# Kernel optimization log

Hardware: AMD Instinct MI355X
Metric: run time of the kernel (lower is better)

The kernel has to match this reference:

```python
import jax, jax.numpy as jnp
import numpy as np

GL16 = [5, 3, 3, 3, 3, 3, 5, 5, 5, 11, 3, 3, 3, 3, 3, 12]  # sum 73
GL7 = [5, 9, 9, 25, 9, 9, 12]  # sum 78
BN_EPS = 1e-5
LRELU_SLOPE = 0.01


def setup_inputs() -> dict:
    key = jax.random.key(0)
    ks = jax.random.split(key, 32)
    B = 65536
    u = lambda k, shp, s: jax.random.uniform(k, shp, minval=-s, maxval=s)
    inp = {}
    inp['x'] = jax.random.normal(ks[0], (B, 310), dtype=jnp.float32)
    # learned adjacency (convert_dis_m(get_ini_dis_m(), 9) placeholder)
    inp['adj'] = jax.random.normal(ks[1], (62, 62), dtype=jnp.float32) * 0.1
    s5 = 1.0 / np.sqrt(5.0)
    inp['lgcn_w'] = u(ks[2], (5, 5), s5)
    inp['lgcn_b'] = u(ks[3], (5,), s5)
    # ChannelAttentionMPL (frequency, C=5) conv1d k=1 weights [out,in]
    inp['ca1_w1'] = jax.random.normal(ks[4], (32, 5)) * 0.3
    inp['ca1_w2'] = jax.random.normal(ks[5], (5, 32)) * 0.1
    # ChannelAttentionMPL (channel, C=62)
    inp['ca2_w1'] = jax.random.normal(ks[6], (32, 62)) * 0.1
    inp['ca2_w2'] = jax.random.normal(ks[7], (62, 32)) * 0.1
    # MesoLayer weights [5,10]
    inp['meso1_w'] = u(ks[8], (5, 10), 1.0 / np.sqrt(78.0))
    inp['meso2_w'] = u(ks[9], (5, 10), 1.0 / np.sqrt(78.0))
    # graphpool.feature_trans index maps (channel gathers into 62 channels)
    inp['idx16'] = jax.random.randint(ks[10], (73,), 0, 62, dtype=jnp.int32)
    inp['idx7'] = jax.random.randint(ks[11], (78,), 0, 62, dtype=jnp.int32)
    # MLP head 735->256->128->64 with eval-mode BatchNorm params
    def lin(ka, kb, fin, fout):
        s = 1.0 / np.sqrt(fin)
        return u(ka, (fin, fout), s), u(kb, (fout,), s)
    inp['w1'], inp['b1'] = lin(ks[12], ks[13], 735, 256)
    inp['w2'], inp['b2'] = lin(ks[14], ks[15], 256, 128)
    inp['w3'], inp['b3'] = lin(ks[16], ks[17], 128, 64)
    for i, (nm, d) in enumerate([('1', 256), ('2', 128), ('3', 64)]):
        inp['g' + nm] = 1.0 + 0.1 * jax.random.normal(ks[18 + 3 * i], (d,))
        inp['be' + nm] = 0.1 * jax.random.normal(ks[19 + 3 * i], (d,))
        inp['m' + nm] = 0.05 * jax.random.normal(ks[20 + 3 * i], (d,))
        inp['v' + nm] = jnp.ones((d,), dtype=jnp.float32)
    return inp


def channel_attention(x, w1, w2):
    # x: [B, C, L]; SE-style attention with avg+max pooling over L
    avg = jnp.mean(x, axis=2)            # [B, C]
    mx = jnp.max(x, axis=2)              # [B, C]
    def mlp(z):
        return jax.nn.relu(z @ w1.T) @ w2.T   # [B, C]
    att = jax.nn.sigmoid(mlp(avg) + mlp(mx))[:, :, None]  # [B, C, 1]
    return x + att * x, att


def meso(feat, idx, weight, graph_list):
    # feat: [B, 62, 5]; gather channels then per-subgraph attention pooling
    f = feat[:, idx]                     # [B, L, 5]
    outs = []
    h = 0
    for n in graph_list:                 # fixed small structural loop
        sub = jax.lax.dynamic_slice_in_dim(f, h, n, axis=1)  # [B, n, 5]
        fw = jnp.einsum('bjg,gh->bjh', sub, weight)          # [B, n, 10]
        # sum_i (fw @ fw^T)[b,j,i] == fw[b,j,:] . sum_i fw[b,i,:]
        scores = jnp.einsum('bjh,bh->bj', fw, jnp.sum(fw, axis=1))  # [B, n]
        att = jax.nn.softmax(scores, axis=1)
        outs.append(jnp.einsum('bj,bjg->bg', att, sub))      # [B, 5]
        h += n
    return jnp.stack(outs, axis=1)       # [B, S, 5]


def _forward(x, adj, lgcn_w, lgcn_b, ca1_w1, ca1_w2, ca2_w1, ca2_w2,
             meso1_w, meso2_w, idx16, idx7,
             w1, b1, g1, be1, m1, v1,
             w2, b2, g2, be2, m2, v2,
             w3, b3, g3, be3, m3, v3):
    B = x.shape[0]
    h = x.reshape(B, 5, 62).transpose(0, 2, 1)                   # [B, 62, 5]
    wf = jnp.einsum('bij,jd->bid', h, lgcn_w)
    h = jnp.einsum('ij,bjd->bid', adj, wf) + lgcn_b              # LocalLayer
    residual = h
    hx = h.transpose(0, 2, 1)                                    # [B, 5, 62]
    x_flat = hx.reshape(B, -1)                                   # [B, 310]
    out, att1 = channel_attention(hx, ca1_w1, ca1_w2)            # [B, 5, 62]
    out, att2 = channel_attention(out.transpose(0, 2, 1), ca2_w1, ca2_w2)  # [B,62,5]
    x1 = meso(residual, idx16, meso1_w, GL16).transpose(0, 2, 1).reshape(B, -1)  # [B, 80]
    x3 = meso(residual, idx7, meso2_w, GL7).transpose(0, 2, 1).reshape(B, -1)    # [B, 35]
    out_flat = out.transpose(0, 2, 1).reshape(B, -1)             # [B, 310]
    cat = jnp.concatenate([x_flat, out_flat, x1, x3], axis=1)    # [B, 735]

    def block(z, w, b, g, be, m, v):
        y = z @ w + b
        y = (y - m) / jnp.sqrt(v + BN_EPS) * g + be              # eval BN
        return jnp.where(y > 0, y, LRELU_SLOPE * y)              # LeakyReLU

    y = block(cat, w1, b1, g1, be1, m1, v1)
    y = block(y, w2, b2, g2, be2, m2, v2)
    y = block(y, w3, b3, g3, be3, m3, v3)
    return y, att1, att2


def reference(x, adj, lgcn_w, lgcn_b, ca1_w1, ca1_w2, ca2_w1, ca2_w2,
              meso1_w, meso2_w, idx16, idx7,
              w1, b1, w2, b2, w3, b3,
              g1, be1, m1, v1, g2, be2, m2, v2, g3, be3, m3, v3):
    return _forward(x, adj, lgcn_w, lgcn_b, ca1_w1, ca1_w2, ca2_w1, ca2_w2,
                    meso1_w, meso2_w, idx16, idx7,
                    w1, b1, g1, be1, m1, v1,
                    w2, b2, g2, be2, m2, v2,
                    w3, b3, g3, be3, m3, v3)
```

## Files before the change

### kernel.cpp

```cpp
#include <hip/hip_runtime.h>
#include <math.h>

#define BN_EPS 1e-5f
#define SLOPE 0.01f

typedef _Float16 f16;
typedef _Float16 f16x8 __attribute__((ext_vector_type(8)));
typedef float f32x4 __attribute__((ext_vector_type(4)));

__device__ __constant__ int c_g16_st[16] = {0,5,8,11,14,17,20,25,30,35,46,49,52,55,58,61};
__device__ __constant__ int c_g16_n[16]  = {5,3,3,3,3,3,5,5,5,11,3,3,3,3,3,12};
__device__ __constant__ int c_g7_st[7]   = {0,5,14,23,48,57,66};
__device__ __constant__ int c_g7_n[7]    = {5,9,9,25,9,9,12};

__device__ __forceinline__ float lrelu(float y) { return y > 0.f ? y : SLOPE * y; }

template<int T, int G, int BASE>
__device__ void meso_part(const int* __restrict__ st_arr, const int* __restrict__ n_arr,
                          int lane, long b, const float* h, const int* __restrict__ idxa,
                          const float* mw, float* fwbuf, float* scbuf,
                          f16* __restrict__ catb)
{
  const int team = lane / T, slot = lane - team * T;
  int st = 0, n = 0;
  if (team < G) { st = st_arr[team]; n = n_arr[team]; }
  float sp[10] = {0,0,0,0,0,0,0,0,0,0};
  if (team < G) {
    for (int j = slot; j < n; j += T) {
      int ri = idxa[st + j];
      float sv[5];
      #pragma unroll
      for (int g = 0; g < 5; ++g) sv[g] = h[ri*8 + g];
      #pragma unroll
      for (int t = 0; t < 10; ++t) {
        float f = sv[0]*mw[t] + sv[1]*mw[10+t] + sv[2]*mw[20+t] + sv[3]*mw[30+t] + sv[4]*mw[40+t];
        fwbuf[(st+j)*10 + t] = f;
        sp[t] += f;
      }
    }
  }
  #pragma unroll
  for (int off = 1; off < T; off <<= 1) {
    #pragma unroll
    for (int t = 0; t < 10; ++t) sp[t] += __shfl_xor(sp[t], off);
  }
  __syncthreads();
  if (team < G) {
    for (int j = slot; j < n; j += T) {
      float sc = 0.f;
      #pragma unroll
      for (int t = 0; t < 10; ++t) sc += fwbuf[(st+j)*10 + t] * sp[t];
      scbuf[st + j] = sc;
    }
  }
  __syncthreads();
  float po[5] = {0,0,0,0,0};
  if (team < G) {
    float mx = -1e30f;
    for (int jj = 0; jj < n; ++jj) mx = fmaxf(mx, scbuf[st + jj]);
    float sum = 0.f;
    for (int jj = 0; jj < n; ++jj) sum += expf(scbuf[st + jj] - mx);
    float inv = 1.f / sum;
    for (int j = slot; j < n; j += T) {
      float a = expf(scbuf[st + j] - mx) * inv;
      int ri = idxa[st + j];
      #pragma unroll
      for (int g = 0; g < 5; ++g) po[g] += a * h[ri*8 + g];
    }
  }
  #pragma unroll
  for (int off = 1; off < T; off <<= 1) {
    #pragma unroll
    for (int g = 0; g < 5; ++g) po[g] += __shfl_xor(po[g], off);
  }
  if (team < G && slot == 0) {
    #pragma unroll
    for (int g = 0; g < 5; ++g) catb[b*736 + BASE + g*G + team] = (f16)po[g];
  }
}

__global__ __launch_bounds__(256) void front_kernel(
    const float* __restrict__ x, const float* __restrict__ adj,
    const float* __restrict__ lgcn_w, const float* __restrict__ lgcn_b,
    const float* __restrict__ ca1_w1, const float* __restrict__ ca1_w2,
    const float* __restrict__ ca2_w1, const float* __restrict__ ca2_w2,
    const float* __restrict__ meso1_w, const float* __restrict__ meso2_w,
    const int* __restrict__ idx16, const int* __restrict__ idx7,
    f16* __restrict__ catb, float* __restrict__ outp, int B)
{
  __shared__ __align__(16) float adjT[62*65];
  __shared__ __align__(16) float wf_s[4][496];
  __shared__ __align__(16) float h_s[4][496];
  __shared__ __align__(16) float fw_s[4][800];
  __shared__ float sc_s[4][80];
  __shared__ float t_s[4][64];
  __shared__ float small_s[4][16];
  __shared__ float v62_s[4][192];
  __shared__ float mw_s[100];

  const int tid = threadIdx.x;
  const int w = tid >> 6;
  const int lane = tid & 63;
  const long b = (long)blockIdx.x * 4 + w;

  for (int t = tid; t < 62*62; t += 256) {
    int i = t / 62, j = t - i*62;
    adjT[j*65 + i] = adj[t];
  }
  if (tid < 50) mw_s[tid] = meso1_w[tid];
  else if (tid < 100) mw_s[tid] = meso2_w[tid - 50];
  __syncthreads();

  const float* xr = x + b * 310;
  if (lane < 62) {
    float wf[5] = {0,0,0,0,0};
    #pragma unroll
    for (int j = 0; j < 5; ++j) {
      float xv = xr[j*62 + lane];
      #pragma unroll
      for (int d = 0; d < 5; ++d) wf[d] += xv * lgcn_w[j*5 + d];
    }
    #pragma unroll
    for (int d = 0; d < 5; ++d) wf_s[w][lane*8 + d] = wf[d];
  }
  __syncthreads();
  if (lane < 62) {
    float acc[5];
    #pragma unroll
    for (int d = 0; d < 5; ++d) acc[d] = lgcn_b[d];
    for (int j = 0; j < 62; ++j) {
      float a = adjT[j*65 + lane];
      float4 w4 = *(const float4*)&wf_s[w][j*8];
      float w5 = wf_s[w][j*8 + 4];
      acc[0] += a*w4.x; acc[1] += a*w4.y; acc[2] += a*w4.z; acc[3] += a*w4.w; acc[4] += a*w5;
    }
    #pragma unroll
    for (int d = 0; d < 5; ++d) h_s[w][lane*8 + d] = acc[d];
  }
  __syncthreads();
  for (int p = lane; p < 310; p += 64) {
    int d = p / 62, i = p - d*62;
    catb[b*736 + p] = (f16)h_s[w][i*8 + d];
  }
  if (lane < 5) {
    float s = 0.f, m = -1e30f;
    for (int i = 0; i < 62; ++i) { float v = h_s[w][i*8 + lane]; s += v; m = fmaxf(m, v); }
    small_s[w][lane] = s * (1.f/62.f);
    small_s[w][5 + lane] = m;
  }
  __syncthreads();
  if (lane < 32) {
    float ta = 0.f, tm = 0.f;
    #pragma unroll
    for (int d = 0; d < 5; ++d) {
      float wv = ca1_w1[lane*5 + d];
      ta += small_s[w][d] * wv;
      tm += small_s[w][5 + d] * wv;
    }
    t_s[w][lane] = fmaxf(ta, 0.f);
    t_s[w][32 + lane] = fmaxf(tm, 0.f);
  }
  __syncthreads();
  if (lane < 5) {
    float sa = 0.f, sm = 0.f;
    for (int o = 0; o < 32; ++o) {
      float wv = ca1_w2[lane*32 + o];
      sa += t_s[w][o] * wv; sm += t_s[w][32 + o] * wv;
    }
    float a = 1.f / (1.f + expf(-(sa + sm)));
    small_s[w][10 + lane] = a;
    outp[(long)B*64 + b*5 + lane] = a;
  }
  __syncthreads();
  if (lane < 62) {
    float s = 0.f, m = -1e30f;
    #pragma unroll
    for (int d = 0; d < 5; ++d) {
      float v = h_s[w][lane*8 + d] * (1.f + small_s[w][10 + d]);
      s += v; m = fmaxf(m, v);
    }
    v62_s[w][lane] = s * (1.f/5.f);
    v62_s[w][64 + lane] = m;
  }
  __syncthreads();
  if (lane < 32) {
    float ta = 0.f, tm = 0.f;
    for (int i = 0; i < 62; ++i) {
      float wv = ca2_w1[lane*62 + i];
      ta += v62_s[w][i] * wv; tm += v62_s[w][64 + i] * wv;
    }
    t_s[w][lane] = fmaxf(ta, 0.f);
    t_s[w][32 + lane] = fmaxf(tm, 0.f);
  }
  __syncthreads();
  if (lane < 62) {
    float sa = 0.f, sm = 0.f;
    for (int o = 0; o < 32; ++o) {
      float wv = ca2_w2[lane*32 + o];
      sa += t_s[w][o] * wv; sm += t_s[w][32 + o] * wv;
    }
    float a = 1.f / (1.f + expf(-(sa + sm)));
    v62_s[w][128 + lane] = a;
    outp[(long)B*69 + b*62 + lane] = a;
  }
  __syncthreads();
  for (int p = lane; p < 310; p += 64) {
    int d = p / 62, i = p - d*62;
    catb[b*736 + 310 + p] = (f16)(h_s[w][i*8 + d] * (1.f + small_s[w][10 + d]) * (1.f + v62_s[w][128 + i]));
  }
  if (lane == 0) catb[b*736 + 735] = (f16)0.f;
  __syncthreads();
  meso_part<4,16,620>(c_g16_st, c_g16_n, lane, b, h_s[w], idx16, mw_s, fw_s[w], sc_s[w], catb);
  __syncthreads();
  meso_part<8,7,700>(c_g7_st, c_g7_n, lane, b, h_s[w], idx7, mw_s + 50, fw_s[w], sc_s[w], catb);
}

__global__ void wcvt_kernel(const float* __restrict__ w1, const float* __restrict__ w2,
                            const float* __restrict__ w3,
                            f16* __restrict__ w1T, f16* __restrict__ w2T, f16* __restrict__ w3T)
{
  int i = blockIdx.x * 256 + threadIdx.x;
  if (i < 256*736) {
    int n = i / 736, k = i - n*736;
    w1T[i] = (f16)(k < 735 ? w1[k*256 + n] : 0.f);
    return;
  }
  int j = i - 256*736;
  if (j < 128*256) {
    int n = j >> 8, k = j & 255;
    w2T[j] = (f16)w2[k*128 + n];
    return;
  }
  int q = j - 128*256;
  if (q < 64*128) {
    int n = q >> 7, k = q & 127;
    w3T[q] = (f16)w3[k*64 + n];
  }
}

__global__ __launch_bounds__(256) void mlp_mfma(
    const f16* __restrict__ cat,
    const f16* __restrict__ w1T, const f16* __restrict__ w2T, const f16* __restrict__ w3T,
    const float* __restrict__ b1, const float* __restrict__ g1, const float* __restrict__ be1,
    const float* __restrict__ m1, const float* __restrict__ v1,
    const float* __restrict__ b2, const float* __restrict__ g2, const float* __restrict__ be2,
    const float* __restrict__ m2, const float* __restrict__ v2,
    const float* __restrict__ b3, const float* __restrict__ g3, const float* __restrict__ be3,
    const float* __restrict__ m3, const float* __restrict__ v3,
    float* __restrict__ outp)
{
  __shared__ __align__(16) f16 a_lds[64*32];
  __shared__ __align__(16) f16 y1s[64*256];
  __shared__ __align__(16) f16 y2s[64*128];

  const int tid = threadIdx.x;
  const int wv = tid >> 6;
  const int lane = tid & 63;
  const int ln = lane & 15;
  const int kg = lane >> 4;
  const long b0 = (long)blockIdx.x * 64;

  f32x4 zero = {0.f, 0.f, 0.f, 0.f};
  f32x4 acc1[4][4];
  #pragma unroll
  for (int i = 0; i < 4; ++i)
    #pragma unroll
    for (int j = 0; j < 4; ++j) acc1[i][j] = zero;

  const int sr  = tid >> 2;
  const int scs = tid & 3;
  const int sdst = sr*64 + ((scs ^ ((sr >> 1) & 3)) << 4);
  const f16* aSrc = cat + (b0 + sr)*736 + scs*8;

  int aoff[4];
  #pragma unroll
  for (int mr = 0; mr < 4; ++mr) {
    int r = mr*16 + ln;
    aoff[mr] = r*64 + ((kg ^ ((r >> 1) & 3)) << 4);
  }

  const f16* w1p[4];
  #pragma unroll
  for (int nc = 0; nc < 4; ++nc)
    w1p[nc] = w1T + (size_t)(wv*64 + nc*16 + ln)*736 + kg*8;

  f16x8 bF[4], bN[4];
  #pragma unroll
  for (int nc = 0; nc < 4; ++nc) bF[nc] = *(const f16x8*)(w1p[nc]);
  f16x8 aReg = *(const f16x8*)(aSrc);
  f16x8 aRegN;

  for (int s = 0; s < 23; ++s) {
    __syncthreads();
    *(f16x8*)((char*)a_lds + sdst) = aReg;
    __syncthreads();
    if (s < 22) {
      aRegN = *(const f16x8*)(aSrc + (s + 1)*32);
      #pragma unroll
      for (int nc = 0; nc < 4; ++nc) bN[nc] = *(const f16x8*)(w1p[nc] + (s + 1)*32);
    }
    #pragma unroll
    for (int mr = 0; mr < 4; ++mr) {
      f16x8 af = *(const f16x8*)((const char*)a_lds + aoff[mr]);
      #pragma unroll
      for (int nc = 0; nc < 4; ++nc)
        acc1[mr][nc] = __builtin_amdgcn_mfma_f32_16x16x32_f16(af, bF[nc], acc1[mr][nc], 0, 0, 0);
    }
    aReg = aRegN;
    #pragma unroll
    for (int nc = 0; nc < 4; ++nc) bF[nc] = bN[nc];
  }

  #pragma unroll
  for (int nc = 0; nc < 4; ++nc) {
    int n = wv*64 + nc*16 + ln;
    float sc = g1[n] * rsqrtf(v1[n] + BN_EPS);
    float bm = b1[n] - m1[n];
    float bo = be1[n];
    int c = n >> 3;
    #pragma unroll
    for (int mr = 0; mr < 4; ++mr) {
      #pragma unroll
      for (int ri = 0; ri < 4; ++ri) {
        int r = mr*16 + kg*4 + ri;
        float y = lrelu((acc1[mr][nc][ri] + bm)*sc + bo);
        int off = r*512 + ((c ^ (r & 7)) << 4) + ((n & 7) << 1);
        *(f16*)((char*)y1s + off) = (f16)y;
      }
    }
  }
  __syncthreads();

  f32x4 acc2[4][2];
  #pragma unroll
  for (int i = 0; i < 4; ++i) { acc2[i][0] = zero; acc2[i][1] = zero; }
  const f16* w2p[2];
  #pragma unroll
  for (int nc = 0; nc < 2; ++nc)
    w2p[nc] = w2T + (size_t)(wv*32 + nc*16 + ln)*256 + kg*8;

  #pragma unroll
  for (int s2 = 0; s2 < 8; ++s2) {
    f16x8 b2f[2];
    #pragma unroll
    for (int nc = 0; nc < 2; ++nc) b2f[nc] = *(const f16x8*)(w2p[nc] + s2*32);
    #pragma unroll
    for (int mr = 0; mr < 4; ++mr) {
      int r = mr*16 + ln;
      int c = s2*4 + kg;
      f16x8 af = *(const f16x8*)((const char*)y1s + r*512 + ((c ^ (r & 7)) << 4));
      #pragma unroll
      for (int nc = 0; nc < 2; ++nc)
        acc2[mr][nc] = __builtin_amdgcn_mfma_f32_16x16x32_f16(af, b2f[nc], acc2[mr][nc], 0, 0, 0);
    }
  }
  #pragma unroll
  for (int nc = 0; nc < 2; ++nc) {
    int n = wv*32 + nc*16 + ln;
    float sc = g2[n] * rsqrtf(v2[n] + BN_EPS);
    float bm = b2[n] - m2[n];
    float bo = be2[n];
    int c = n >> 3;
    #pragma unroll
    for (int mr = 0; mr < 4; ++mr) {
      #pragma unroll
      for (int ri = 0; ri < 4; ++ri) {
        int r = mr*16 + kg*4 + ri;
        float y = lrelu((acc2[mr][nc][ri] + bm)*sc + bo);
        int off = r*256 + ((c ^ (r & 7)) << 4) + ((n & 7) << 1);
        *(f16*)((char*)y2s + off) = (f16)y;
      }
    }
  }
  __syncthreads();

  f32x4 acc3[4];
  #pragma unroll
  for (int i = 0; i < 4; ++i) acc3[i] = zero;
  const f16* w3p = w3T + (size_t)(wv*16 + ln)*128 + kg*8;

  #pragma unroll
  for (int s3 = 0; s3 < 4; ++s3) {
    f16x8 bf = *(const f16x8*)(w3p + s3*32);
    #pragma unroll
    for (int mr = 0; mr < 4; ++mr) {
      int r = mr*16 + ln;
      int c = s3*4 + kg;
      f16x8 af = *(const f16x8*)((const char*)y2s + r*256 + ((c ^ (r & 7)) << 4));
      acc3[mr] = __builtin_amdgcn_mfma_f32_16x16x32_f16(af, bf, acc3[mr], 0, 0, 0);
    }
  }
  {
    int n = wv*16 + ln;
    float sc = g3[n] * rsqrtf(v3[n] + BN_EPS);
    float bm = b3[n] - m3[n];
    float bo = be3[n];
    #pragma unroll
    for (int mr = 0; mr < 4; ++mr) {
      #pragma unroll
      for (int ri = 0; ri < 4; ++ri) {
        int r = mr*16 + kg*4 + ri;
        float y = lrelu((acc3[mr][ri] + bm)*sc + bo);
        outp[(size_t)(b0 + r)*64 + n] = y;
      }
    }
  }
}

extern "C" void kernel_launch(void* const* d_in, const int* in_sizes, int n_in,
                              void* d_out, int out_size, void* d_ws, size_t ws_size,
                              hipStream_t stream) {
  const float* x       = (const float*)d_in[0];
  const float* adj     = (const float*)d_in[1];
  const float* lgcn_w  = (const float*)d_in[2];
  const float* lgcn_b  = (const float*)d_in[3];
  const float* ca1_w1  = (const float*)d_in[4];
  const float* ca1_w2  = (const float*)d_in[5];
  const float* ca2_w1  = (const float*)d_in[6];
  const float* ca2_w2  = (const float*)d_in[7];
  const float* meso1_w = (const float*)d_in[8];
  const float* meso2_w = (const float*)d_in[9];
  const int*   idx16   = (const int*)d_in[10];
  const int*   idx7    = (const int*)d_in[11];
  const float* w1 = (const float*)d_in[12];
  const float* b1 = (const float*)d_in[13];
  const float* w2 = (const float*)d_in[14];
  const float* b2 = (const float*)d_in[15];
  const float* w3 = (const float*)d_in[16];
  const float* b3 = (const float*)d_in[17];
  const float* g1 = (const float*)d_in[18];
  const float* be1= (const float*)d_in[19];
  const float* m1 = (const float*)d_in[20];
  const float* v1 = (const float*)d_in[21];
  const float* g2 = (const float*)d_in[22];
  const float* be2= (const float*)d_in[23];
  const float* m2 = (const float*)d_in[24];
  const float* v2 = (const float*)d_in[25];
  const float* g3 = (const float*)d_in[26];
  const float* be3= (const float*)d_in[27];
  const float* m3 = (const float*)d_in[28];
  const float* v3 = (const float*)d_in[29];

  const int B = in_sizes[0] / 310;

  const size_t catBytes = (size_t)B * 736 * sizeof(f16);
  char* wsc = (char*)d_ws;
  f16* catb = (f16*)wsc;
  f16* w1T  = (f16*)(wsc + catBytes);
  f16* w2T  = (f16*)(wsc + catBytes + 256*736*sizeof(f16));
  f16* w3T  = (f16*)(wsc + catBytes + (256*736 + 128*256)*sizeof(f16));
  const size_t need = catBytes + (256*736 + 128*256 + 64*128)*sizeof(f16);
  if (ws_size < need) return;

  wcvt_kernel<<<(256*736 + 128*256 + 64*128 + 255)/256, 256, 0, stream>>>(w1, w2, w3, w1T, w2T, w3T);
  front_kernel<<<B/4, 256, 0, stream>>>(x, adj, lgcn_w, lgcn_b, ca1_w1, ca1_w2,
                                        ca2_w1, ca2_w2, meso1_w, meso2_w,
                                        idx16, idx7, catb, (float*)d_out, B);
  mlp_mfma<<<B/64, 256, 0, stream>>>(catb, w1T, w2T, w3T,
                                     b1, g1, be1, m1, v1,
                                     b2, g2, be2, m2, v2,
                                     b3, g3, be3, m3, v3, (float*)d_out);
}
```

Measured before the change: 702.0 us.

## Fold graph conv into Kronecker weight matrix and compute via MFMA GEMM

Folds the adjacency and lgcn_w products into one 310x310 (padded to 320) fp16 matrix built in the prep kernel. The graph-convolution output is then computed for 64 rows per block with MFMA 16x16x32 in a new gemm_h kernel, which writes it into the cat buffer. The remaining front kernel reads h back from the cat buffer at fp16 precision and parallelises the pooling reductions and the ca2 first layer across more lanes. This replaces scalar per-row FMAs with matrix-core work, at the cost of an extra kernel launch, a round trip through global memory, and fp16 rounding of x and of h before attention.

Result: faster. 640.7 us (-8.7%).

```diff
diff --git a/kernel.cpp b/kernel.cpp
--- a/kernel.cpp
+++ b/kernel.cpp
@@ -79,17 +79,141 @@
   }
 }
 
-__global__ __launch_bounds__(256) void front_kernel(
-    const float* __restrict__ x, const float* __restrict__ adj,
-    const float* __restrict__ lgcn_w, const float* __restrict__ lgcn_b,
+__global__ void wcvt_kernel(const float* __restrict__ w1, const float* __restrict__ w2,
+                            const float* __restrict__ w3,
+                            const float* __restrict__ adj, const float* __restrict__ lgcn_w,
+                            f16* __restrict__ w1T, f16* __restrict__ w2T, f16* __restrict__ w3T,
+                            f16* __restrict__ Mp)
+{
+  int i = blockIdx.x * 256 + threadIdx.x;
+  if (i < 256*736) {
+    int n = i / 736, k = i - n*736;
+    w1T[i] = (f16)(k < 735 ? w1[k*256 + n] : 0.f);
+    return;
+  }
+  int j = i - 256*736;
+  if (j < 128*256) {
+    int n = j >> 8, k = j & 255;
+    w2T[j] = (f16)w2[k*128 + n];
+    return;
+  }
+  int q = j - 128*256;
+  if (q < 64*128) {
+    int n = q >> 7, k = q & 127;
+    w3T[q] = (f16)w3[k*64 + n];
+    return;
+  }
+  int m = q - 64*128;
+  if (m < 320*320) {
+    int col = m / 320, k = m - col*320;
+    float v = 0.f;
+    if (col < 310 && k < 310) {
+      int d = col / 62, ii = col - d*62;
+      int g = k / 62,  jj = k - g*62;
+      v = adj[ii*62 + jj] * lgcn_w[g*5 + d];
+    }
+    Mp[m] = (f16)v;
+  }
+}
+
+__global__ __launch_bounds__(256) void gemm_h(
+    const float* __restrict__ x, const f16* __restrict__ Mp,
+    const float* __restrict__ lgcn_b, f16* __restrict__ catb)
+{
+  __shared__ __align__(16) f16 a_lds[64*320];
+
+  const int tid = threadIdx.x;
+  const int wv = tid >> 6;
+  const int lane = tid & 63;
+  const int ln = lane & 15;
+  const int kg = lane >> 4;
+  const long b0 = (long)blockIdx.x * 64;
+
+  const f16* mp[5];
+  #pragma unroll
+  for (int nc = 0; nc < 5; ++nc)
+    mp[nc] = Mp + (size_t)(wv*80 + nc*16 + ln)*320 + kg*8;
+  f16x8 bF[5], bN[5];
+  #pragma unroll
+  for (int nc = 0; nc < 5; ++nc) bF[nc] = *(const f16x8*)(mp[nc]);
+
+  for (int rr = 0; rr < 16; ++rr) {
+    int row = wv*16 + rr;
+    if (lane < 8) {
+      int c = 38 + (lane >> 2);
+      *(unsigned*)((char*)a_lds + row*640 + ((c ^ (row & 7)) << 4) + (lane & 3)*4) = 0u;
+    }
+    const float* xr = x + (b0 + row)*310;
+    for (int f = lane; f < 155; f += 64) {
+      float2 v = *(const float2*)(xr + 2*f);
+      int k = 2*f;
+      int c = k >> 3;
+      f16 h0 = (f16)v.x, h1 = (f16)v.y;
+      unsigned u = (unsigned)*(unsigned short*)&h0 | ((unsigned)*(unsigned short*)&h1 << 16);
+      *(unsigned*)((char*)a_lds + row*640 + ((c ^ (row & 7)) << 4) + (k & 7)*2) = u;
+    }
+  }
+  __syncthreads();
+
+  f32x4 zero = {0.f, 0.f, 0.f, 0.f};
+  f32x4 acc[4][5];
+  #pragma unroll
+  for (int mr = 0; mr < 4; ++mr)
+    #pragma unroll
+    for (int nc = 0; nc < 5; ++nc) acc[mr][nc] = zero;
+
+  for (int s = 0; s < 10; ++s) {
+    if (s < 9) {
+      #pragma unroll
+      for (int nc = 0; nc < 5; ++nc) bN[nc] = *(const f16x8*)(mp[nc] + (s + 1)*32);
+    }
+    #pragma unroll
+    for (int mr = 0; mr < 4; ++mr) {
+      int r = mr*16 + ln;
+      int c = s*4 + kg;
+      f16x8 af = *(const f16x8*)((const char*)a_lds + r*640 + ((c ^ (r & 7)) << 4));
+      #pragma unroll
+      for (int nc = 0; nc < 5; ++nc)
+        acc[mr][nc] = __builtin_amdgcn_mfma_f32_16x16x32_f16(af, bF[nc], acc[mr][nc], 0, 0, 0);
+    }
+    #pragma unroll
+    for (int nc = 0; nc < 5; ++nc) bF[nc] = bN[nc];
+  }
+
+  __syncthreads();
+  #pragma unroll
+  for (int nc = 0; nc < 5; ++nc) {
+    int n = wv*80 + nc*16 + ln;
+    float bias = (n < 310) ? lgcn_b[n / 62] : 0.f;
+    int c = n >> 3;
+    #pragma unroll
+    for (int mr = 0; mr < 4; ++mr) {
+      #pragma unroll
+      for (int ri = 0; ri < 4; ++ri) {
+        int r = mr*16 + kg*4 + ri;
+        f16 val = (f16)(acc[mr][nc][ri] + bias);
+        *(f16*)((char*)a_lds + r*640 + ((c ^ (r & 7)) << 4) + (n & 7)*2) = val;
+      }
+    }
+  }
+  __syncthreads();
+  for (int rr = 0; rr < 16; ++rr) {
+    int row = wv*16 + rr;
+    if (lane < 39) {
+      int c = lane;
+      f16x8 v = *(const f16x8*)((const char*)a_lds + row*640 + ((c ^ (row & 7)) << 4));
+      *(f16x8*)(catb + (b0 + row)*736 + c*8) = v;
+    }
+  }
+}
+
+__global__ __launch_bounds__(256) void front2(
     const float* __restrict__ ca1_w1, const float* __restrict__ ca1_w2,
     const float* __restrict__ ca2_w1, const float* __restrict__ ca2_w2,
     const float* __restrict__ meso1_w, const float* __restrict__ meso2_w,
     const int* __restrict__ idx16, const int* __restrict__ idx7,
     f16* __restrict__ catb, float* __restrict__ outp, int B)
 {
-  __shared__ __align__(16) float adjT[62*65];
-  __shared__ __align__(16) float wf_s[4][496];
   __shared__ __align__(16) float h_s[4][496];
   __shared__ __align__(16) float fw_s[4][800];
   __shared__ float sc_s[4][80];
@@ -103,50 +227,35 @@
   const int lane = tid & 63;
   const long b = (long)blockIdx.x * 4 + w;
 
-  for (int t = tid; t < 62*62; t += 256) {
-    int i = t / 62, j = t - i*62;
-    adjT[j*65 + i] = adj[t];
-  }
   if (tid < 50) mw_s[tid] = meso1_w[tid];
   else if (tid < 100) mw_s[tid] = meso2_w[tid - 50];
-  __syncthreads();
-
-  const float* xr = x + b * 310;
-  if (lane < 62) {
-    float wf[5] = {0,0,0,0,0};
-    #pragma unroll
-    for (int j = 0; j < 5; ++j) {
-      float xv = xr[j*62 + lane];
-      #pragma unroll
-      for (int d = 0; d < 5; ++d) wf[d] += xv * lgcn_w[j*5 + d];
-    }
-    #pragma unroll
-    for (int d = 0; d < 5; ++d) wf_s[w][lane*8 + d] = wf[d];
-  }
-  __syncthreads();
-  if (lane < 62) {
-    float acc[5];
-    #pragma unroll
-    for (int d = 0; d < 5; ++d) acc[d] = lgcn_b[d];
-    for (int j = 0; j < 62; ++j) {
-      float a = adjT[j*65 + lane];
-      float4 w4 = *(const float4*)&wf_s[w][j*8];
-      float w5 = wf_s[w][j*8 + 4];
-      acc[0] += a*w4.x; acc[1] += a*w4.y; acc[2] += a*w4.z; acc[3] += a*w4.w; acc[4] += a*w5;
-    }
-    #pragma unroll
-    for (int d = 0; d < 5; ++d) h_s[w][lane*8 + d] = acc[d];
-  }
-  __syncthreads();
+
   for (int p = lane; p < 310; p += 64) {
+    float v = (float)catb[b*736 + p];
     int d = p / 62, i = p - d*62;
-    catb[b*736 + p] = (f16)h_s[w][i*8 + d];
-  }
-  if (lane < 5) {
+    h_s[w][i*8 + d] = v;
+  }
+  __syncthreads();
+
+  {
+    int d = lane >> 3, q = lane & 7;
     float s = 0.f, m = -1e30f;
-    for (int i = 0; i < 62; ++i) { float v = h_s[w][i*8 + lane]; s += v; m = fmaxf(m, v); }
-    small_s[w][lane] = s * (1.f/62.f);
-    small_s[w][5 + lane] = m;
+    if (d < 5) {
+      #pragma unroll
+      for (int e = 0; e < 8; ++e) {
+        int i = q*8 + e;
+        if (i < 62) { float v = h_s[w][i*8 + d]; s += v; m = fmaxf(m, v); }
+      }
+    }
+    #pragma unroll
+    for (int off = 1; off < 8; off <<= 1) {
+      s += __shfl_xor(s, off);
+      m = fmaxf(m, __shfl_xor(m, off));
+    }
+    if (d < 5 && q == 0) {
+      small_s[w][d] = s * (1.f/62.f);
+      small_s[w][5 + d] = m;
+    }
   }
   __syncthreads();
   if (lane < 32) {
@@ -183,14 +292,13 @@
     v62_s[w][64 + lane] = m;
   }
   __syncthreads();
-  if (lane < 32) {
-    float ta = 0.f, tm = 0.f;
-    for (int i = 0; i < 62; ++i) {
-      float wv = ca2_w1[lane*62 + i];
-      ta += v62_s[w][i] * wv; tm += v62_s[w][64 + i] * wv;
-    }
-    t_s[w][lane] = fmaxf(ta, 0.f);
-    t_s[w][32 + lane] = fmaxf(tm, 0.f);
+  {
+    int half = lane >> 5;
+    int o = lane & 31;
+    const float* src = &v62_s[w][half*64];
+    float t = 0.f;
+    for (int i = 0; i < 62; ++i) t += src[i] * ca2_w1[o*62 + i];
+    t_s[w][half*32 + o] = fmaxf(t, 0.f);
   }
   __syncthreads();
   if (lane < 62) {
@@ -213,29 +321,6 @@
   meso_part<4,16,620>(c_g16_st, c_g16_n, lane, b, h_s[w], idx16, mw_s, fw_s[w], sc_s[w], catb);
   __syncthreads();
   meso_part<8,7,700>(c_g7_st, c_g7_n, lane, b, h_s[w], idx7, mw_s + 50, fw_s[w], sc_s[w], catb);
-}
-
-__global__ void wcvt_kernel(const float* __restrict__ w1, const float* __restrict__ w2,
-                            const float* __restrict__ w3,
-                            f16* __restrict__ w1T, f16* __restrict__ w2T, f16* __restrict__ w3T)
-{
-  int i = blockIdx.x * 256 + threadIdx.x;
-  if (i < 256*736) {
-    int n = i / 736, k = i - n*736;
-    w1T[i] = (f16)(k < 735 ? w1[k*256 + n] : 0.f);
-    return;
-  }
-  int j = i - 256*736;
-  if (j < 128*256) {
-    int n = j >> 8, k = j & 255;
-    w2T[j] = (f16)w2[k*128 + n];
-    return;
-  }
-  int q = j - 128*256;
-  if (q < 64*128) {
-    int n = q >> 7, k = q & 127;
-    w3T[q] = (f16)w3[k*64 + n];
-  }
 }
 
 __global__ __launch_bounds__(256) void mlp_mfma(
@@ -449,13 +534,16 @@
   f16* w1T  = (f16*)(wsc + catBytes);
   f16* w2T  = (f16*)(wsc + catBytes + 256*736*sizeof(f16));
   f16* w3T  = (f16*)(wsc + catBytes + (256*736 + 128*256)*sizeof(f16));
-  const size_t need = catBytes + (256*736 + 128*256 + 64*128)*sizeof(f16);
+  f16* Mp   = (f16*)(wsc + catBytes + (256*736 + 128*256 + 64*128)*sizeof(f16));
+  const size_t need = catBytes + (256*736 + 128*256 + 64*128 + 320*320)*sizeof(f16);
   if (ws_size < need) return;
 
-  wcvt_kernel<<<(256*736 + 128*256 + 64*128 + 255)/256, 256, 0, stream>>>(w1, w2, w3, w1T, w2T, w3T);
-  front_kernel<<<B/4, 256, 0, stream>>>(x, adj, lgcn_w, lgcn_b, ca1_w1, ca1_w2,
-                                        ca2_w1, ca2_w2, meso1_w, meso2_w,
-                                        idx16, idx7, catb, (float*)d_out, B);
+  const int prepElems = 256*736 + 128*256 + 64*128 + 320*320;
+  wcvt_kernel<<<(prepElems + 255)/256, 256, 0, stream>>>(w1, w2, w3, adj, lgcn_w,
+                                                         w1T, w2T, w3T, Mp);
+  gemm_h<<<B/64, 256, 0, stream>>>(x, Mp, lgcn_b, catb);
+  front2<<<B/4, 256, 0, stream>>>(ca1_w1, ca1_w2, ca2_w1, ca2_w2, meso1_w, meso2_w,
+                                  idx16, idx7, catb, (float*)d_out, B);
   mlp_mfma<<<B/64, 256, 0, stream>>>(catb, w1T, w2T, w3T,
                                      b1, g1, be1, m1, v1,
                                      b2, g2, be2, m2, v2,
```
